# Optimization experiments

Measured on AMD Instinct MI355X. Metric: run time of the kernel, lower is better.

## Reference

```python
import jax, jax.numpy as jnp
import numpy as np
import math

B, T, C = 4, 2048, 768
N_HEADS = 12

def setup_inputs() -> dict:
    key = jax.random.key(0)
    k1, k2, k3 = jax.random.split(key, 3)
    s_in = 1.0 / math.sqrt(C)
    x = jax.random.normal(k1, (B, T, C), dtype=jnp.float32)
    w_attn = jax.random.normal(k2, (C, 3 * C), dtype=jnp.float32) * s_in
    b_attn = jnp.zeros((3 * C,), dtype=jnp.float32)
    w_proj = jax.random.normal(k3, (C, C), dtype=jnp.float32) * s_in
    b_proj = jnp.zeros((C,), dtype=jnp.float32)
    return {"x": x, "w_attn": w_attn, "b_attn": b_attn, "w_proj": w_proj, "b_proj": b_proj}

def reference(x, w_attn, b_attn, w_proj, b_proj):
    Bx, Tx, Cx = x.shape
    hd = Cx // N_HEADS  # head_dim
    qkv = x @ w_attn + b_attn                       # [B,T,3C]
    q, k, v = jnp.split(qkv, 3, axis=-1)
    def heads(t):  # [B,T,C] -> [B,H,T,hd]
        return t.reshape(Bx, Tx, N_HEADS, hd).transpose(0, 2, 1, 3)
    q, k, v = heads(q), heads(k), heads(v)
    scores = jnp.einsum('bhqd,bhkd->bhqk', q, k) * (1.0 / math.sqrt(hd))
    causal = jnp.tril(jnp.ones((Tx, Tx), dtype=bool))
    scores = jnp.where(causal, scores, -jnp.inf)
    attn = jax.nn.softmax(scores, axis=-1)
    out = jnp.einsum('bhqk,bhkd->bhqd', attn, v)    # [B,H,T,hd]
    out = out.transpose(0, 2, 1, 3).reshape(Bx, Tx, Cx)
    return out @ w_proj + b_proj
```

## Files before the change

kernel.cpp:

```cpp
#include <hip/hip_runtime.h>
#include <hip/hip_bf16.h>

typedef __bf16 bf16_8 __attribute__((ext_vector_type(8)));
typedef float f32x4 __attribute__((ext_vector_type(4)));
typedef unsigned short us4 __attribute__((ext_vector_type(4)));

#define AS1(p) ((const __attribute__((address_space(1))) void*)(p))
#define AS3(p) ((__attribute__((address_space(3))) void*)(p))

#define Bb 4
#define Tt 2048
#define Cc 768
#define NH 12
#define HD 64
#define Mrows 8192
#define N1 2304
#define KDIM 768
#define QSCALE 0.1803368801111204f
#define THR 10.0f

__device__ __forceinline__ unsigned short bfbits(float x) {
    __bf16 h = (__bf16)x;
    return __builtin_bit_cast(unsigned short, h);
}

__device__ __forceinline__ float exp2fast(float x) {
#if __has_builtin(__builtin_amdgcn_exp2f)
    return __builtin_amdgcn_exp2f(x);
#else
    return __expf(0.6931471805599453f * x);
#endif
}

__global__ __launch_bounds__(256) void cast_f32_bf16(const float* __restrict__ in,
                                                     __bf16* __restrict__ out, int n4) {
    int i = blockIdx.x * blockDim.x + threadIdx.x;
    if (i < n4) {
        float4 v = ((const float4*)in)[i];
        us4 o;
        o.x = bfbits(v.x); o.y = bfbits(v.y); o.z = bfbits(v.z); o.w = bfbits(v.w);
        *(us4*)(out + (size_t)i * 4) = o;
    }
}

__global__ __launch_bounds__(256) void transpose_cast(const float* __restrict__ in,
                                                      __bf16* __restrict__ out, int R, int Cn) {
    __shared__ float tile[32][33];
    int c0 = blockIdx.x * 32, r0 = blockIdx.y * 32;
    int tx = threadIdx.x, ty = threadIdx.y;
#pragma unroll
    for (int i = 0; i < 4; ++i)
        tile[ty + i * 8][tx] = in[(size_t)(r0 + ty + i * 8) * Cn + c0 + tx];
    __syncthreads();
#pragma unroll
    for (int i = 0; i < 4; ++i)
        out[(size_t)(c0 + ty + i * 8) * R + r0 + tx] = (__bf16)tile[tx][ty + i * 8];
}

template <int MODE>
__global__ __launch_bounds__(256) void gemm_bt(const __bf16* __restrict__ A,
                                               const __bf16* __restrict__ Bt,
                                               const float* __restrict__ bias,
                                               float* __restrict__ outf,
                                               __bf16* __restrict__ qb,
                                               __bf16* __restrict__ kb,
                                               __bf16* __restrict__ vTb,
                                               int M, int N, int K) {
    __shared__ __bf16 As[2][128 * 64];
    __shared__ __bf16 Bs[2][128 * 64];
    int tid = threadIdx.x;
    int w = tid >> 6, l = tid & 63, lr = l & 15, lg = l >> 4;
    int wm = w >> 1, wn = w & 1;

    int gx = gridDim.x, gy = gridDim.y;
    int nwg = gx * gy;
    int orig = blockIdx.y * gx + blockIdx.x;
    int q8 = nwg >> 3, r8 = nwg & 7;
    int xcd = orig & 7, rest = orig >> 3;
    int swz = (xcd < r8) ? xcd * (q8 + 1) + rest
                         : r8 * (q8 + 1) + (xcd - r8) * q8 + rest;
    int bx = swz / gy, by = swz % gy;
    int m0 = bx * 128, n0 = by * 128;

    f32x4 acc[4][4] = {};

#define GSTAGE(buf, kk) do {                                                                 \
    _Pragma("unroll")                                                                        \
    for (int i_ = 0; i_ < 4; ++i_) {                                                         \
        int c_ = i_ * 256 + tid;                                                             \
        int row_ = c_ >> 3;                                                                  \
        int jc_ = ((c_ & 7) ^ (row_ & 7)) << 3;                                              \
        __builtin_amdgcn_global_load_lds(AS1(A + (size_t)(m0 + row_) * K + (kk) + jc_),      \
                                         AS3(&As[buf][c_ * 8]), 16, 0, 0);                   \
        __builtin_amdgcn_global_load_lds(AS1(Bt + (size_t)(n0 + row_) * K + (kk) + jc_),     \
                                         AS3(&Bs[buf][c_ * 8]), 16, 0, 0);                   \
    }                                                                                        \
} while (0)

    GSTAGE(0, 0);
    asm volatile("s_waitcnt vmcnt(0)" ::: "memory");
    __builtin_amdgcn_sched_barrier(0);
    __builtin_amdgcn_s_barrier();
    __builtin_amdgcn_sched_barrier(0);

    int nkt = K >> 6;
    for (int kt = 0; kt < nkt; ++kt) {
        int cur = kt & 1;
        if (kt + 1 < nkt) {
            GSTAGE(cur ^ 1, (kt + 1) * 64);
            asm volatile("s_waitcnt vmcnt(8)" ::: "memory");
        } else {
            asm volatile("s_waitcnt vmcnt(0)" ::: "memory");
        }
        __builtin_amdgcn_sched_barrier(0);
        __builtin_amdgcn_s_barrier();
        __builtin_amdgcn_sched_barrier(0);

        const __bf16* Ac = &As[cur][0];
        const __bf16* Bc = &Bs[cur][0];
        bf16_8 af[4][2], bfr[4][2];
#pragma unroll
        for (int mi = 0; mi < 4; ++mi)
#pragma unroll
            for (int ks = 0; ks < 2; ++ks)
                af[mi][ks] = *(const bf16_8*)&Ac[(wm * 64 + mi * 16 + lr) * 64 +
                                                 (((ks * 4 + lg) ^ (lr & 7)) << 3)];
#pragma unroll
        for (int ni = 0; ni < 4; ++ni)
#pragma unroll
            for (int ks = 0; ks < 2; ++ks)
                bfr[ni][ks] = *(const bf16_8*)&Bc[(wn * 64 + ni * 16 + lr) * 64 +
                                                  (((ks * 4 + lg) ^ (lr & 7)) << 3)];
#pragma unroll
        for (int mi = 0; mi < 4; ++mi)
#pragma unroll
            for (int ni = 0; ni < 4; ++ni)
#pragma unroll
                for (int ks = 0; ks < 2; ++ks)
                    acc[mi][ni] = __builtin_amdgcn_mfma_f32_16x16x32_bf16(af[mi][ks], bfr[ni][ks],
                                                                          acc[mi][ni], 0, 0, 0);
        asm volatile("s_waitcnt lgkmcnt(0)" ::: "memory");
        __builtin_amdgcn_sched_barrier(0);
        __builtin_amdgcn_s_barrier();
        __builtin_amdgcn_sched_barrier(0);
    }

#pragma unroll
    for (int ni = 0; ni < 4; ++ni) {
        int gn = n0 + wn * 64 + ni * 16 + lr;
        float bv = bias[gn];
#pragma unroll
        for (int mi = 0; mi < 4; ++mi) {
            int gm0 = m0 + wm * 64 + mi * 16 + lg * 4;
            f32x4 v = acc[mi][ni];
            if (MODE == 1) {
#pragma unroll
                for (int r = 0; r < 4; ++r)
                    outf[(size_t)(gm0 + r) * N + gn] = v[r] + bv;
            } else {
                int seg = gn / Cc;
                int rem = gn - seg * Cc;
                int h = rem >> 6, d = rem & 63;
                int b = gm0 >> 11, t = gm0 & 2047;
                size_t bh = (size_t)b * NH + h;
                if (seg < 2) {
                    float sc = (seg == 0) ? QSCALE : 1.0f;
                    __bf16* dst = (seg ? kb : qb) + (bh * Tt + t) * HD + d;
#pragma unroll
                    for (int r = 0; r < 4; ++r)
                        dst[(size_t)r * HD] = (__bf16)((v[r] + bv) * sc);
                } else {
                    us4 pk;
#pragma unroll
                    for (int r = 0; r < 4; ++r) pk[r] = bfbits(v[r] + bv);
                    *(us4*)(vTb + (bh * HD + d) * Tt + t) = pk;
                }
            }
        }
    }
}

__global__ __launch_bounds__(256, 2) void attn_fwd(const __bf16* __restrict__ q,
                                                   const __bf16* __restrict__ k,
                                                   const __bf16* __restrict__ vT,
                                                   __bf16* __restrict__ aout) {
    __shared__ __bf16 Ks[2][64 * 64];
    __shared__ __bf16 Vs[2][64 * 64];
    __shared__ __bf16 Ps[4][16 * 64];
    const float NEGINF = -__builtin_inff();

    int blk = blockIdx.x;
    int bh = blk % 48;
    int j = blk / 48;
    int qtA = j, qtB = 31 - j;
    int tid = threadIdx.x;
    int w = tid >> 6, l = tid & 63, lr = l & 15, lg = l >> 4;

    const __bf16* qp = q + (size_t)bh * Tt * HD;
    const __bf16* kp = k + (size_t)bh * Tt * HD;
    const __bf16* vp = vT + (size_t)bh * HD * Tt;

    bf16_8 qfA0, qfA1, qfB0, qfB1;
    {
        int q0A = qtA * 64 + w * 16, q0B = qtB * 64 + w * 16;
        qfA0 = *(const bf16_8*)(qp + (size_t)(q0A + lr) * HD + lg * 8);
        qfA1 = *(const bf16_8*)(qp + (size_t)(q0A + lr) * HD + 32 + lg * 8);
        qfB0 = *(const bf16_8*)(qp + (size_t)(q0B + lr) * HD + lg * 8);
        qfB1 = *(const bf16_8*)(qp + (size_t)(q0B + lr) * HD + 32 + lg * 8);
    }

    f32x4 accOA[4] = {}, accOB[4] = {};
    float mA[4], mB[4], sA[4] = {}, sB[4] = {};
#pragma unroll
    for (int r = 0; r < 4; ++r) { mA[r] = NEGINF; mB[r] = NEGINF; }

    const int swz = lr & 7;
    const int co0 = (lg ^ swz) * 8;
    const int co1 = ((4 + lg) ^ swz) * 8;
    const int qloc = w * 16 + lg * 4;
    __bf16* Pw = &Ps[w][0];

#define STAGE(buf, kvbase) do {                                                              \
    int c0_ = tid, c1_ = 256 + tid;                                                          \
    int row0_ = c0_ >> 3, j0_ = (c0_ & 7) ^ (row0_ & 7);                                     \
    int row1_ = c1_ >> 3, j1_ = (c1_ & 7) ^ (row1_ & 7);                                     \
    __builtin_amdgcn_global_load_lds(AS1(kp + (size_t)((kvbase) + row0_) * HD + j0_ * 8),    \
                                     AS3(&Ks[buf][c0_ * 8]), 16, 0, 0);                      \
    __builtin_amdgcn_global_load_lds(AS1(vp + (size_t)row0_ * Tt + (kvbase) + j0_ * 8),      \
                                     AS3(&Vs[buf][c0_ * 8]), 16, 0, 0);                      \
    __builtin_amdgcn_global_load_lds(AS1(kp + (size_t)((kvbase) + row1_) * HD + j1_ * 8),    \
                                     AS3(&Ks[buf][c1_ * 8]), 16, 0, 0);                      \
    __builtin_amdgcn_global_load_lds(AS1(vp + (size_t)row1_ * Tt + (kvbase) + j1_ * 8),      \
                                     AS3(&Vs[buf][c1_ * 8]), 16, 0, 0);                      \
} while (0)

#define TILE_COMPUTE(qf0, qf1, accO, m, s, diag) do {                                        \
    f32x4 accS_[4] = {};                                                                     \
    __builtin_amdgcn_s_setprio(1);                                                           \
    _Pragma("unroll")                                                                        \
    for (int nt = 0; nt < 4; ++nt) {                                                         \
        int rb = (nt * 16 + lr) * 64;                                                        \
        bf16_8 kf0_ = *(const bf16_8*)(Kc_ + rb + co0);                                      \
        bf16_8 kf1_ = *(const bf16_8*)(Kc_ + rb + co1);                                      \
        accS_[nt] = __builtin_amdgcn_mfma_f32_16x16x32_bf16(qf0, kf0_, accS_[nt], 0, 0, 0);  \
        accS_[nt] = __builtin_amdgcn_mfma_f32_16x16x32_bf16(qf1, kf1_, accS_[nt], 0, 0, 0);  \
    }                                                                                        \
    __builtin_amdgcn_s_setprio(0);                                                           \
    if (diag) {                                                                              \
        _Pragma("unroll")                                                                    \
        for (int nt = 0; nt < 4; ++nt) {                                                     \
            int kloc_ = nt * 16 + lr;                                                        \
            _Pragma("unroll")                                                                \
            for (int r = 0; r < 4; ++r)                                                      \
                if (kloc_ > qloc + r) accS_[nt][r] = NEGINF;                                 \
        }                                                                                    \
    }                                                                                        \
    float lm_[4];                                                                            \
    _Pragma("unroll")                                                                        \
    for (int r = 0; r < 4; ++r)                                                              \
        lm_[r] = fmaxf(fmaxf(accS_[0][r], accS_[1][r]), fmaxf(accS_[2][r], accS_[3][r]));    \
    bool cond_ = (lm_[0] <= m[0] + THR) && (lm_[1] <= m[1] + THR) &&                         \
                 (lm_[2] <= m[2] + THR) && (lm_[3] <= m[3] + THR);                           \
    if (!__all(cond_)) {                                                                     \
        _Pragma("unroll")                                                                    \
        for (int r = 0; r < 4; ++r) {                                                        \
            float mx_ = lm_[r];                                                              \
            _Pragma("unroll")                                                                \
            for (int off = 1; off < 16; off <<= 1)                                           \
                mx_ = fmaxf(mx_, __shfl_xor(mx_, off));                                      \
            float mnew_ = fmaxf(m[r], mx_);                                                  \
            float al_ = exp2fast(m[r] - mnew_);                                              \
            m[r] = mnew_;                                                                    \
            s[r] *= al_;                                                                     \
            _Pragma("unroll")                                                                \
            for (int dt = 0; dt < 4; ++dt) accO[dt][r] *= al_;                               \
        }                                                                                    \
    }                                                                                        \
    _Pragma("unroll")                                                                        \
    for (int r = 0; r < 4; ++r) {                                                            \
        int prow_ = lg * 4 + r;                                                              \
        _Pragma("unroll")                                                                    \
        for (int nt = 0; nt < 4; ++nt) {                                                     \
            float pv_ = exp2fast(accS_[nt][r] - m[r]);                                       \
            s[r] += pv_;                                                                     \
            int col_ = nt * 16 + lr;                                                         \
            Pw[prow_ * 64 + (((col_ >> 3) ^ (prow_ & 7)) << 3) + (col_ & 7)] = (__bf16)pv_;  \
        }                                                                                    \
    }                                                                                        \
    bf16_8 pf0_ = *(const bf16_8*)&Pw[lr * 64 + ((lg ^ swz) << 3)];                          \
    bf16_8 pf1_ = *(const bf16_8*)&Pw[lr * 64 + (((4 + lg) ^ swz) << 3)];                    \
    __builtin_amdgcn_s_setprio(1);                                                           \
    _Pragma("unroll")                                                                        \
    for (int dt = 0; dt < 4; ++dt) {                                                         \
        int rb = (dt * 16 + lr) * 64;                                                        \
        bf16_8 vf0_ = *(const bf16_8*)(Vc_ + rb + co0);                                      \
        bf16_8 vf1_ = *(const bf16_8*)(Vc_ + rb + co1);                                      \
        accO[dt] = __builtin_amdgcn_mfma_f32_16x16x32_bf16(pf0_, vf0_, accO[dt], 0, 0, 0);   \
        accO[dt] = __builtin_amdgcn_mfma_f32_16x16x32_bf16(pf1_, vf1_, accO[dt], 0, 0, 0);   \
    }                                                                                        \
    __builtin_amdgcn_s_setprio(0);                                                           \
} while (0)

    STAGE(0, 0);
    asm volatile("s_waitcnt vmcnt(0)" ::: "memory");
    __builtin_amdgcn_sched_barrier(0);
    __builtin_amdgcn_s_barrier();
    __builtin_amdgcn_sched_barrier(0);

    for (int kv = 0; kv <= qtB; ++kv) {
        int cur = kv & 1;
        if (kv < qtB) {
            STAGE(cur ^ 1, (kv + 1) * 64);
            asm volatile("s_waitcnt vmcnt(4)" ::: "memory");
        } else {
            asm volatile("s_waitcnt vmcnt(0)" ::: "memory");
        }
        __builtin_amdgcn_sched_barrier(0);
        __builtin_amdgcn_s_barrier();
        __builtin_amdgcn_sched_barrier(0);

        const __bf16* Kc_ = &Ks[cur][0];
        const __bf16* Vc_ = &Vs[cur][0];
        TILE_COMPUTE(qfB0, qfB1, accOB, mB, sB, kv == qtB);
        if (kv <= qtA)
            TILE_COMPUTE(qfA0, qfA1, accOA, mA, sA, kv == qtA);

        asm volatile("s_waitcnt lgkmcnt(0)" ::: "memory");
        __builtin_amdgcn_sched_barrier(0);
        __builtin_amdgcn_s_barrier();
        __builtin_amdgcn_sched_barrier(0);
    }

    int b = bh / NH, h = bh - b * NH;
#define EPILOGUE(accO, s, qt) do {                                                           \
    _Pragma("unroll")                                                                        \
    for (int r = 0; r < 4; ++r) {                                                            \
        float ss_ = s[r];                                                                    \
        _Pragma("unroll")                                                                    \
        for (int off = 1; off < 16; off <<= 1)                                               \
            ss_ += __shfl_xor(ss_, off);                                                     \
        float inv_ = 1.0f / ss_;                                                             \
        size_t row_ = (size_t)(b * Tt + (qt) * 64 + w * 16 + lg * 4 + r) * Cc + h * HD;      \
        _Pragma("unroll")                                                                    \
        for (int dt = 0; dt < 4; ++dt)                                                       \
            aout[row_ + dt * 16 + lr] = (__bf16)(accO[dt][r] * inv_);                        \
    }                                                                                        \
} while (0)

    EPILOGUE(accOA, sA, qtA);
    EPILOGUE(accOB, sB, qtB);
}

extern "C" void kernel_launch(void* const* d_in, const int* in_sizes, int n_in,
                              void* d_out, int out_size, void* d_ws, size_t ws_size,
                              hipStream_t stream) {
    const float* x      = (const float*)d_in[0];
    const float* w_attn = (const float*)d_in[1];
    const float* b_attn = (const float*)d_in[2];
    const float* w_proj = (const float*)d_in[3];
    const float* b_proj = (const float*)d_in[4];
    float* out = (float*)d_out;

    char* ws = (char*)d_ws;
    constexpr size_t SZ_XB   = (size_t)Mrows * KDIM * 2;
    constexpr size_t SZ_WAT  = (size_t)N1 * KDIM * 2;
    constexpr size_t SZ_WPT  = (size_t)Cc * Cc * 2;
    constexpr size_t SZ_HEAD = (size_t)Bb * NH * Tt * HD * 2;
    __bf16* xb  = (__bf16*)ws;
    __bf16* wat = (__bf16*)(ws + SZ_XB);
    __bf16* wpt = (__bf16*)(ws + SZ_XB + SZ_WAT);
    __bf16* qb  = (__bf16*)(ws + SZ_XB + SZ_WAT + SZ_WPT);
    __bf16* kb  = (__bf16*)(ws + SZ_XB + SZ_WAT + SZ_WPT + SZ_HEAD);
    __bf16* vTb = (__bf16*)(ws + SZ_XB + SZ_WAT + SZ_WPT + 2 * SZ_HEAD);
    __bf16* ao  = (__bf16*)(ws + SZ_XB + SZ_WAT + SZ_WPT + 3 * SZ_HEAD);

    cast_f32_bf16<<<(Mrows * KDIM / 4 + 255) / 256, 256, 0, stream>>>(x, xb, Mrows * KDIM / 4);
    transpose_cast<<<dim3(N1 / 32, KDIM / 32), dim3(32, 8), 0, stream>>>(w_attn, wat, KDIM, N1);
    transpose_cast<<<dim3(Cc / 32, Cc / 32), dim3(32, 8), 0, stream>>>(w_proj, wpt, Cc, Cc);

    gemm_bt<0><<<dim3(Mrows / 128, N1 / 128), 256, 0, stream>>>(
        xb, wat, b_attn, nullptr, qb, kb, vTb, Mrows, N1, KDIM);

    attn_fwd<<<48 * 16, 256, 0, stream>>>(qb, kb, vTb, ao);

    gemm_bt<1><<<dim3(Mrows / 128, Cc / 128), 256, 0, stream>>>(
        ao, wpt, b_proj, out, nullptr, nullptr, nullptr, Mrows, Cc, KDIM);
}
```

Baseline: 136.9 us.

## Fuse the two query tiles' attention compute to share K/V fragment loads

Replaces the two sequential per-query-tile compute calls with a fused TILE_AB path, used while both tiles are active, plus a B-only path for the rest. The fused path reads each K and V fragment from LDS once and feeds both query tiles' MFMAs, interleaved for more independent work. P is given a separate LDS buffer per tile, and launch bounds are raised from 2 to 3 blocks per CU. The cost is more live registers, which the 3-block bound may squeeze into spills, and more LDS per block. An unused leftover SM_TAIL macro is also added.

```diff
diff --git a/kernel.cpp b/kernel.cpp
--- a/kernel.cpp
+++ b/kernel.cpp
@@ -180,13 +180,13 @@
     }
 }
 
-__global__ __launch_bounds__(256, 2) void attn_fwd(const __bf16* __restrict__ q,
+__global__ __launch_bounds__(256, 3) void attn_fwd(const __bf16* __restrict__ q,
                                                    const __bf16* __restrict__ k,
                                                    const __bf16* __restrict__ vT,
                                                    __bf16* __restrict__ aout) {
     __shared__ __bf16 Ks[2][64 * 64];
     __shared__ __bf16 Vs[2][64 * 64];
-    __shared__ __bf16 Ps[4][16 * 64];
+    __shared__ __bf16 Ps[4][2][16 * 64];
     const float NEGINF = -__builtin_inff();
 
     int blk = blockIdx.x;
@@ -218,7 +218,8 @@
     const int co0 = (lg ^ swz) * 8;
     const int co1 = ((4 + lg) ^ swz) * 8;
     const int qloc = w * 16 + lg * 4;
-    __bf16* Pw = &Ps[w][0];
+    __bf16* PwA = &Ps[w][0][0];
+    __bf16* PwB = &Ps[w][1][0];
 
 #define STAGE(buf, kvbase) do {                                                              \
     int c0_ = tid, c1_ = 256 + tid;                                                          \
@@ -234,27 +235,7 @@
                                      AS3(&Vs[buf][c1_ * 8]), 16, 0, 0);                      \
 } while (0)
 
-#define TILE_COMPUTE(qf0, qf1, accO, m, s, diag) do {                                        \
-    f32x4 accS_[4] = {};                                                                     \
-    __builtin_amdgcn_s_setprio(1);                                                           \
-    _Pragma("unroll")                                                                        \
-    for (int nt = 0; nt < 4; ++nt) {                                                         \
-        int rb = (nt * 16 + lr) * 64;                                                        \
-        bf16_8 kf0_ = *(const bf16_8*)(Kc_ + rb + co0);                                      \
-        bf16_8 kf1_ = *(const bf16_8*)(Kc_ + rb + co1);                                      \
-        accS_[nt] = __builtin_amdgcn_mfma_f32_16x16x32_bf16(qf0, kf0_, accS_[nt], 0, 0, 0);  \
-        accS_[nt] = __builtin_amdgcn_mfma_f32_16x16x32_bf16(qf1, kf1_, accS_[nt], 0, 0, 0);  \
-    }                                                                                        \
-    __builtin_amdgcn_s_setprio(0);                                                           \
-    if (diag) {                                                                              \
-        _Pragma("unroll")                                                                    \
-        for (int nt = 0; nt < 4; ++nt) {                                                     \
-            int kloc_ = nt * 16 + lr;                                                        \
-            _Pragma("unroll")                                                                \
-            for (int r = 0; r < 4; ++r)                                                      \
-                if (kloc_ > qloc + r) accS_[nt][r] = NEGINF;                                 \
-        }                                                                                    \
-    }                                                                                        \
+#define SM_TAIL(accS_, m, s, Pw) do {                                                        \
     float lm_[4];                                                                            \
     _Pragma("unroll")                                                                        \
     for (int r = 0; r < 4; ++r)                                                              \
@@ -273,7 +254,51 @@
             m[r] = mnew_;                                                                    \
             s[r] *= al_;                                                                     \
             _Pragma("unroll")                                                                \
-            for (int dt = 0; dt < 4; ++dt) accO[dt][r] *= al_;                               \
+            for (int dt = 0; dt < 4; ++dt) acc##O_OF_##accS_                                 \
+        }                                                                                    \
+    }                                                                                        \
+} while (0)
+
+
+#define TILE_B(diag) do {                                                                    \
+    f32x4 aSB_[4] = {};                                                                      \
+    __builtin_amdgcn_s_setprio(1);                                                           \
+    _Pragma("unroll")                                                                        \
+    for (int nt = 0; nt < 4; ++nt) {                                                         \
+        int rb = (nt * 16 + lr) * 64;                                                        \
+        bf16_8 kf0_ = *(const bf16_8*)(Kc_ + rb + co0);                                      \
+        bf16_8 kf1_ = *(const bf16_8*)(Kc_ + rb + co1);                                      \
+        aSB_[nt] = __builtin_amdgcn_mfma_f32_16x16x32_bf16(qfB0, kf0_, aSB_[nt], 0, 0, 0);   \
+        aSB_[nt] = __builtin_amdgcn_mfma_f32_16x16x32_bf16(qfB1, kf1_, aSB_[nt], 0, 0, 0);   \
+    }                                                                                        \
+    __builtin_amdgcn_s_setprio(0);                                                           \
+    if (diag) {                                                                              \
+        _Pragma("unroll")                                                                    \
+        for (int nt = 0; nt < 4; ++nt) {                                                     \
+            int kloc_ = nt * 16 + lr;                                                        \
+            _Pragma("unroll")                                                                \
+            for (int r = 0; r < 4; ++r)                                                      \
+                if (kloc_ > qloc + r) aSB_[nt][r] = NEGINF;                                  \
+        }                                                                                    \
+    }                                                                                        \
+    float lm_[4];                                                                            \
+    _Pragma("unroll")                                                                        \
+    for (int r = 0; r < 4; ++r)                                                              \
+        lm_[r] = fmaxf(fmaxf(aSB_[0][r], aSB_[1][r]), fmaxf(aSB_[2][r], aSB_[3][r]));        \
+    bool cond_ = (lm_[0] <= mB[0] + THR) && (lm_[1] <= mB[1] + THR) &&                       \
+                 (lm_[2] <= mB[2] + THR) && (lm_[3] <= mB[3] + THR);                         \
+    if (!__all(cond_)) {                                                                     \
+        _Pragma("unroll")                                                                    \
+        for (int r = 0; r < 4; ++r) {                                                        \
+            float mx_ = lm_[r];                                                              \
+            _Pragma("unroll")                                                                \
+            for (int off = 1; off < 16; off <<= 1)                                           \
+                mx_ = fmaxf(mx_, __shfl_xor(mx_, off));                                      \
+            float mnew_ = fmaxf(mB[r], mx_);                                                 \
+            float al_ = exp2fast(mB[r] - mnew_);                                             \
+            mB[r] = mnew_; sB[r] *= al_;                                                     \
+            _Pragma("unroll")                                                                \
+            for (int dt = 0; dt < 4; ++dt) accOB[dt][r] *= al_;                              \
         }                                                                                    \
     }                                                                                        \
     _Pragma("unroll")                                                                        \
@@ -281,22 +306,115 @@
         int prow_ = lg * 4 + r;                                                              \
         _Pragma("unroll")                                                                    \
         for (int nt = 0; nt < 4; ++nt) {                                                     \
-            float pv_ = exp2fast(accS_[nt][r] - m[r]);                                       \
-            s[r] += pv_;                                                                     \
+            float pv_ = exp2fast(aSB_[nt][r] - mB[r]);                                       \
+            sB[r] += pv_;                                                                    \
             int col_ = nt * 16 + lr;                                                         \
-            Pw[prow_ * 64 + (((col_ >> 3) ^ (prow_ & 7)) << 3) + (col_ & 7)] = (__bf16)pv_;  \
-        }                                                                                    \
-    }                                                                                        \
-    bf16_8 pf0_ = *(const bf16_8*)&Pw[lr * 64 + ((lg ^ swz) << 3)];                          \
-    bf16_8 pf1_ = *(const bf16_8*)&Pw[lr * 64 + (((4 + lg) ^ swz) << 3)];                    \
+            PwB[prow_ * 64 + (((col_ >> 3) ^ (prow_ & 7)) << 3) + (col_ & 7)] = (__bf16)pv_; \
+        }                                                                                    \
+    }                                                                                        \
+    bf16_8 pfB0_ = *(const bf16_8*)&PwB[lr * 64 + ((lg ^ swz) << 3)];                        \
+    bf16_8 pfB1_ = *(const bf16_8*)&PwB[lr * 64 + (((4 + lg) ^ swz) << 3)];                  \
     __builtin_amdgcn_s_setprio(1);                                                           \
     _Pragma("unroll")                                                                        \
     for (int dt = 0; dt < 4; ++dt) {                                                         \
         int rb = (dt * 16 + lr) * 64;                                                        \
         bf16_8 vf0_ = *(const bf16_8*)(Vc_ + rb + co0);                                      \
         bf16_8 vf1_ = *(const bf16_8*)(Vc_ + rb + co1);                                      \
-        accO[dt] = __builtin_amdgcn_mfma_f32_16x16x32_bf16(pf0_, vf0_, accO[dt], 0, 0, 0);   \
-        accO[dt] = __builtin_amdgcn_mfma_f32_16x16x32_bf16(pf1_, vf1_, accO[dt], 0, 0, 0);   \
+        accOB[dt] = __builtin_amdgcn_mfma_f32_16x16x32_bf16(pfB0_, vf0_, accOB[dt], 0, 0, 0);\
+        accOB[dt] = __builtin_amdgcn_mfma_f32_16x16x32_bf16(pfB1_, vf1_, accOB[dt], 0, 0, 0);\
+    }                                                                                        \
+    __builtin_amdgcn_s_setprio(0);                                                           \
+} while (0)
+
+#define TILE_AB(diagA) do {                                                                  \
+    f32x4 aSA_[4] = {}, aSB_[4] = {};                                                        \
+    __builtin_amdgcn_s_setprio(1);                                                           \
+    _Pragma("unroll")                                                                        \
+    for (int nt = 0; nt < 4; ++nt) {                                                         \
+        int rb = (nt * 16 + lr) * 64;                                                        \
+        bf16_8 kf0_ = *(const bf16_8*)(Kc_ + rb + co0);                                      \
+        bf16_8 kf1_ = *(const bf16_8*)(Kc_ + rb + co1);                                      \
+        aSB_[nt] = __builtin_amdgcn_mfma_f32_16x16x32_bf16(qfB0, kf0_, aSB_[nt], 0, 0, 0);   \
+        aSA_[nt] = __builtin_amdgcn_mfma_f32_16x16x32_bf16(qfA0, kf0_, aSA_[nt], 0, 0, 0);   \
+        aSB_[nt] = __builtin_amdgcn_mfma_f32_16x16x32_bf16(qfB1, kf1_, aSB_[nt], 0, 0, 0);   \
+        aSA_[nt] = __builtin_amdgcn_mfma_f32_16x16x32_bf16(qfA1, kf1_, aSA_[nt], 0, 0, 0);   \
+    }                                                                                        \
+    __builtin_amdgcn_s_setprio(0);                                                           \
+    if (diagA) {                                                                             \
+        _Pragma("unroll")                                                                    \
+        for (int nt = 0; nt < 4; ++nt) {                                                     \
+            int kloc_ = nt * 16 + lr;                                                        \
+            _Pragma("unroll")                                                                \
+            for (int r = 0; r < 4; ++r)                                                      \
+                if (kloc_ > qloc + r) aSA_[nt][r] = NEGINF;                                  \
+        }                                                                                    \
+    }                                                                                        \
+    float lmA_[4], lmB_[4];                                                                  \
+    _Pragma("unroll")                                                                        \
+    for (int r = 0; r < 4; ++r) {                                                            \
+        lmA_[r] = fmaxf(fmaxf(aSA_[0][r], aSA_[1][r]), fmaxf(aSA_[2][r], aSA_[3][r]));       \
+        lmB_[r] = fmaxf(fmaxf(aSB_[0][r], aSB_[1][r]), fmaxf(aSB_[2][r], aSB_[3][r]));       \
+    }                                                                                        \
+    bool condA_ = (lmA_[0] <= mA[0] + THR) && (lmA_[1] <= mA[1] + THR) &&                    \
+                  (lmA_[2] <= mA[2] + THR) && (lmA_[3] <= mA[3] + THR);                      \
+    if (!__all(condA_)) {                                                                    \
+        _Pragma("unroll")                                                                    \
+        for (int r = 0; r < 4; ++r) {                                                        \
+            float mx_ = lmA_[r];                                                             \
+            _Pragma("unroll")                                                                \
+            for (int off = 1; off < 16; off <<= 1)                                           \
+                mx_ = fmaxf(mx_, __shfl_xor(mx_, off));                                      \
+            float mnew_ = fmaxf(mA[r], mx_);                                                 \
+            float al_ = exp2fast(mA[r] - mnew_);                                             \
+            mA[r] = mnew_; sA[r] *= al_;                                                     \
+            _Pragma("unroll")                                                                \
+            for (int dt = 0; dt < 4; ++dt) accOA[dt][r] *= al_;                              \
+        }                                                                                    \
+    }                                                                                        \
+    bool condB_ = (lmB_[0] <= mB[0] + THR) && (lmB_[1] <= mB[1] + THR) &&                    \
+                  (lmB_[2] <= mB[2] + THR) && (lmB_[3] <= mB[3] + THR);                      \
+    if (!__all(condB_)) {                                                                    \
+        _Pragma("unroll")                                                                    \
+        for (int r = 0; r < 4; ++r) {                                                        \
+            float mx_ = lmB_[r];                                                             \
+            _Pragma("unroll")                                                                \
+            for (int off = 1; off < 16; off <<= 1)                                           \
+                mx_ = fmaxf(mx_, __shfl_xor(mx_, off));                                      \
+            float mnew_ = fmaxf(mB[r], mx_);                                                 \
+            float al_ = exp2fast(mB[r] - mnew_);                                             \
+            mB[r] = mnew_; sB[r] *= al_;                                                     \
+            _Pragma("unroll")                                                                \
+            for (int dt = 0; dt < 4; ++dt) accOB[dt][r] *= al_;                              \
+        }                                                                                    \
+    }                                                                                        \
+    _Pragma("unroll")                                                                        \
+    for (int r = 0; r < 4; ++r) {                                                            \
+        int prow_ = lg * 4 + r;                                                              \
+        _Pragma("unroll")                                                                    \
+        for (int nt = 0; nt < 4; ++nt) {                                                     \
+            int col_ = nt * 16 + lr;                                                         \
+            int off_ = prow_ * 64 + (((col_ >> 3) ^ (prow_ & 7)) << 3) + (col_ & 7);         \
+            float pvA_ = exp2fast(aSA_[nt][r] - mA[r]);                                      \
+            float pvB_ = exp2fast(aSB_[nt][r] - mB[r]);                                      \
+            sA[r] += pvA_; sB[r] += pvB_;                                                    \
+            PwA[off_] = (__bf16)pvA_;                                                        \
+            PwB[off_] = (__bf16)pvB_;                                                        \
+        }                                                                                    \
+    }                                                                                        \
+    bf16_8 pfA0_ = *(const bf16_8*)&PwA[lr * 64 + ((lg ^ swz) << 3)];                        \
+    bf16_8 pfA1_ = *(const bf16_8*)&PwA[lr * 64 + (((4 + lg) ^ swz) << 3)];                  \
+    bf16_8 pfB0_ = *(const bf16_8*)&PwB[lr * 64 + ((lg ^ swz) << 3)];                        \
+    bf16_8 pfB1_ = *(const bf16_8*)&PwB[lr * 64 + (((4 + lg) ^ swz) << 3)];                  \
+    __builtin_amdgcn_s_setprio(1);                                                           \
+    _Pragma("unroll")                                                                        \
+    for (int dt = 0; dt < 4; ++dt) {                                                         \
+        int rb = (dt * 16 + lr) * 64;                                                        \
+        bf16_8 vf0_ = *(const bf16_8*)(Vc_ + rb + co0);                                      \
+        bf16_8 vf1_ = *(const bf16_8*)(Vc_ + rb + co1);                                      \
+        accOB[dt] = __builtin_amdgcn_mfma_f32_16x16x32_bf16(pfB0_, vf0_, accOB[dt], 0, 0, 0);\
+        accOA[dt] = __builtin_amdgcn_mfma_f32_16x16x32_bf16(pfA0_, vf0_, accOA[dt], 0, 0, 0);\
+        accOB[dt] = __builtin_amdgcn_mfma_f32_16x16x32_bf16(pfB1_, vf1_, accOB[dt], 0, 0, 0);\
+        accOA[dt] = __builtin_amdgcn_mfma_f32_16x16x32_bf16(pfA1_, vf1_, accOA[dt], 0, 0, 0);\
     }                                                                                        \
     __builtin_amdgcn_s_setprio(0);                                                           \
 } while (0)
@@ -321,9 +439,10 @@
 
         const __bf16* Kc_ = &Ks[cur][0];
         const __bf16* Vc_ = &Vs[cur][0];
-        TILE_COMPUTE(qfB0, qfB1, accOB, mB, sB, kv == qtB);
         if (kv <= qtA)
-            TILE_COMPUTE(qfA0, qfA1, accOA, mA, sA, kv == qtA);
+            TILE_AB(kv == qtA);
+        else
+            TILE_B(kv == qtB);
 
         asm volatile("s_waitcnt lgkmcnt(0)" ::: "memory");
         __builtin_amdgcn_sched_barrier(0);
```

After: 234.3 us. +71.1%, slower.
